# Kernel tuning notes

Measured on AMD Instinct MI355X. Metric: run time of the kernel, lower is better.

The kernel has to match this reference:

```python
import jax, jax.numpy as jnp
import numpy as np

B, T, D, K = 4, 4096, 384, 64

def setup_inputs() -> dict:
    key = jax.random.key(0)
    k1, k2, k3, k4 = jax.random.split(key, 4)
    x = jax.random.normal(k1, (B, T, D), dtype=jnp.float32)
    # nn.Linear weights stored as (out_features, in_features); y = x @ W.T
    Wk = jax.random.normal(k2, (K, D), dtype=jnp.float32) * (1.0 / np.sqrt(D))
    Wq = jax.random.normal(k3, (K, D), dtype=jnp.float32) * (1.0 / np.sqrt(D))
    Wv = jax.random.normal(k4, (D, D), dtype=jnp.float32) * (1.0 / np.sqrt(D))
    return {"x": x, "Wk": Wk, "Wq": Wq, "Wv": Wv}

def reference(x, Wk, Wq, Wv):
    # x: (B,T,D)
    k = jnp.einsum('btd,kd->btk', x, Wk)   # (B,T,K)
    q = jnp.einsum('btd,kd->btk', x, Wq)   # (B,T,K)
    v = jnp.einsum('btd,ed->bte', x, Wv)   # (B,T,D)
    scores = jnp.einsum('btk,bsk->bts', q, k)  # (B,T,T)
    Tq = x.shape[1]
    causal = jnp.tril(jnp.ones((Tq, Tq), dtype=bool))[None, :, :]
    scores = jnp.where(causal, scores, -jnp.inf)
    w = jax.nn.softmax(scores / jnp.sqrt(jnp.asarray(Wk.shape[0], scores.dtype)), axis=-1)
    return jnp.einsum('bts,bsd->btd', w, v)  # (B,T,D)
```

## Files before the change

### kernel.cpp

```cpp
#include <hip/hip_runtime.h>


#define BB 4
#define TT 4096
#define DD 384

#define OWKA 0
#define OWQA 24576
#define OWVB 49152
#define OYK  196608
#define OYQ  1245184
#define OVT  2293760

#define C_EXP 0.18033688011112042f

typedef __bf16 bf16x8 __attribute__((ext_vector_type(8)));
typedef float f32x16 __attribute__((ext_vector_type(16)));
typedef unsigned short u16x4 __attribute__((ext_vector_type(4)));

__device__ __forceinline__ unsigned short f2bf(float f) {
  unsigned int u = __builtin_bit_cast(unsigned int, f);
  u += 0x7FFFu + ((u >> 16) & 1u);
  return (unsigned short)(u >> 16);
}

__device__ __forceinline__ bf16x8 ldb8(const unsigned short* p) {
  return *reinterpret_cast<const bf16x8*>(p);
}

__global__ __launch_bounds__(256) void convert_w(
    const float* __restrict__ Wk, const float* __restrict__ Wq,
    const float* __restrict__ Wv, unsigned short* __restrict__ ws) {
  int g = blockIdx.x * 256 + threadIdx.x;
  int row = g / 96;
  int fin = (g - row * 96) * 4;
  const float* src;
  unsigned short* dstbase;
  int m;
  if (row < 64)       { src = Wk + row * 384;         dstbase = ws + OWKA; m = row; }
  else if (row < 128) { src = Wq + (row - 64) * 384;  dstbase = ws + OWQA; m = row - 64; }
  else                { src = Wv + (row - 128) * 384; dstbase = ws + OWVB; m = row - 128; }
  float4 f = *reinterpret_cast<const float4*>(src + fin);
  u16x4 o;
  o[0] = f2bf(f.x); o[1] = f2bf(f.y); o[2] = f2bf(f.z); o[3] = f2bf(f.w);
  unsigned short* dst = dstbase + (m >> 5) * 12288 + (fin >> 4) * 512
                        + ((((fin >> 3) & 1) << 5) + (m & 31)) * 8 + (fin & 7);
  *reinterpret_cast<u16x4*>(dst) = o;
}

__global__ __launch_bounds__(512) void proj_fused(
    const float* __restrict__ x, const unsigned short* __restrict__ ws_r,
    unsigned short* __restrict__ Yk, unsigned short* __restrict__ Yq,
    unsigned short* __restrict__ Vt) {
  __shared__ __align__(16) unsigned short xlds[24576];
  int tb = blockIdx.x;
  int b = tb >> 6;
  int tid = threadIdx.x;
  {
    int r = tid >> 3, e = tid & 7;
    const float* xr = x + (tb * 64 + r) * DD + e * 48;
#pragma unroll
    for (int i = 0; i < 12; i++) {
      int fin = e * 48 + i * 4;
      float4 f = *reinterpret_cast<const float4*>(xr + i * 4);
      u16x4 o;
      o[0] = f2bf(f.x); o[1] = f2bf(f.y); o[2] = f2bf(f.z); o[3] = f2bf(f.w);
      unsigned short* dst = xlds + (r >> 5) * 12288 + (fin >> 4) * 512
                            + ((((fin >> 3) & 1) << 5) + (r & 31)) * 8 + (fin & 7);
      *reinterpret_cast<u16x4*>(dst) = o;
    }
  }
  __syncthreads();
  int wid = tid >> 6, lane = tid & 63;
  int l31 = lane & 31, h8 = lane >> 5;
  const f32x16 fz16 = {};
  if (wid < 2) {
    const unsigned short* Wa = ws_r + (wid ? OWQA : OWKA) + lane * 8;
    unsigned short* Ysel = (wid ? Yq : Yk);
    f32x16 acc[2][2];
    acc[0][0] = fz16; acc[0][1] = fz16; acc[1][0] = fz16; acc[1][1] = fz16;
    for (int ks = 0; ks < 24; ks++) {
      bf16x8 a0 = ldb8(Wa + ks * 512);
      bf16x8 a1 = ldb8(Wa + 12288 + ks * 512);
      bf16x8 b0 = ldb8(xlds + ks * 512 + lane * 8);
      bf16x8 b1 = ldb8(xlds + 12288 + ks * 512 + lane * 8);
      acc[0][0] = __builtin_amdgcn_mfma_f32_32x32x16_bf16(a0, b0, acc[0][0], 0, 0, 0);
      acc[0][1] = __builtin_amdgcn_mfma_f32_32x32x16_bf16(a0, b1, acc[0][1], 0, 0, 0);
      acc[1][0] = __builtin_amdgcn_mfma_f32_32x32x16_bf16(a1, b0, acc[1][0], 0, 0, 0);
      acc[1][1] = __builtin_amdgcn_mfma_f32_32x32x16_bf16(a1, b1, acc[1][1], 0, 0, 0);
    }
#pragma unroll
    for (int mt = 0; mt < 2; mt++)
#pragma unroll
      for (int nt = 0; nt < 2; nt++) {
        int tile = b * 128 + (tb & 63) * 2 + nt;
#pragma unroll
        for (int rg = 0; rg < 4; rg++) {
          u16x4 o;
#pragma unroll
          for (int i = 0; i < 4; i++) o[i] = f2bf(acc[mt][nt][rg * 4 + i]);
          *reinterpret_cast<u16x4*>(Ysel + tile * 2048 + (mt * 2 + (rg >> 1)) * 512
                                    + (((rg & 1) << 5) + l31) * 8 + 4 * h8) = o;
        }
      }
  } else {
    int vw = wid - 2;
    const unsigned short* Wb = ws_r + OWVB + vw * 2 * 12288 + lane * 8;
    f32x16 acc[2][2];
    acc[0][0] = fz16; acc[0][1] = fz16; acc[1][0] = fz16; acc[1][1] = fz16;
    for (int ks = 0; ks < 24; ks++) {
      bf16x8 a0 = ldb8(xlds + ks * 512 + lane * 8);
      bf16x8 a1 = ldb8(xlds + 12288 + ks * 512 + lane * 8);
      bf16x8 w0 = ldb8(Wb + ks * 512);
      bf16x8 w1 = ldb8(Wb + 12288 + ks * 512);
      acc[0][0] = __builtin_amdgcn_mfma_f32_32x32x16_bf16(a0, w0, acc[0][0], 0, 0, 0);
      acc[0][1] = __builtin_amdgcn_mfma_f32_32x32x16_bf16(a0, w1, acc[0][1], 0, 0, 0);
      acc[1][0] = __builtin_amdgcn_mfma_f32_32x32x16_bf16(a1, w0, acc[1][0], 0, 0, 0);
      acc[1][1] = __builtin_amdgcn_mfma_f32_32x32x16_bf16(a1, w1, acc[1][1], 0, 0, 0);
    }
    int k128 = (tb & 63) >> 1;
#pragma unroll
    for (int t32 = 0; t32 < 2; t32++)
#pragma unroll
      for (int dt = 0; dt < 2; dt++) {
        int dti = vw * 2 + dt;
        unsigned short* vbase = Vt + ((b * 12 + dti) * 32 + k128) * 4096;
#pragma unroll
        for (int rg = 0; rg < 4; rg++) {
          u16x4 o;
#pragma unroll
          for (int i = 0; i < 4; i++) o[i] = f2bf(acc[t32][dt][rg * 4 + i]);
          int kseg = 4 * (tb & 1) + t32 * 2 + (rg >> 1);
          *reinterpret_cast<u16x4*>(vbase + kseg * 512
                                    + (((rg & 1) << 5) + l31) * 8 + 4 * h8) = o;
        }
      }
  }
}

__global__ __launch_bounds__(512, 2) void flash_attn(
    const unsigned short* __restrict__ Yk, const unsigned short* __restrict__ Yq,
    const unsigned short* __restrict__ Vt, float* __restrict__ out) {
  __shared__ __align__(16) unsigned short pbuf[2][2][8192];
  int blk = blockIdx.x;
  int xcd = blk & 7;
  int b = xcd >> 1, half = xcd & 1;
  int n = blk >> 3;
  int st = (n < 32) ? (127 - 2 * n - half) : (2 * (n - 32) + half);
  int tid = threadIdx.x;
  int wid = tid >> 6, lane = tid & 63;
  int g = wid >> 2, wg = wid & 3;
  int l31 = lane & 31, h8 = lane >> 5;
  const f32x16 fz16 = {};
  const unsigned short* qbase = Yq + (b * 128 + st) * 2048 + lane * 8;
  bf16x8 qf[4];
#pragma unroll
  for (int ks = 0; ks < 4; ks++) qf[ks] = ldb8(qbase + ks * 512);
  f32x16 acc[3];
  acc[0] = fz16; acc[1] = fz16; acc[2] = fz16;
  float psum = 0.f;
  int n128 = (st >> 2) + 1;
  int W = (n128 + 1) >> 1;
  int qrow = st * 32 + l31;
  const unsigned short* kbase = Yk + (b * 128 + wg) * 2048 + lane * 8;
  const unsigned short* vbase = Vt + ((b * 12 + wg * 3) * 32) * 4096 + lane * 8;
#pragma unroll 1
  for (int it = 0; it < W; it++) {
    int kb = 2 * it + g;
    int kbc = (kb < n128) ? kb : (n128 - 1);
    const unsigned short* kt = kbase + kbc * 8192;
    bf16x8 kf[4];
#pragma unroll
    for (int ks = 0; ks < 4; ks++) kf[ks] = ldb8(kt + ks * 512);
    f32x16 sacc = fz16;
#pragma unroll
    for (int ks = 0; ks < 4; ks++)
      sacc = __builtin_amdgcn_mfma_f32_32x32x16_bf16(kf[ks], qf[ks], sacc, 0, 0, 0);
    int kg0 = kb * 128 + wg * 32 + 4 * h8;
    unsigned short* pw = pbuf[g][it & 1];
#pragma unroll
    for (int rg = 0; rg < 4; rg++) {
      u16x4 o;
#pragma unroll
      for (int i = 0; i < 4; i++) {
        int key = kg0 + rg * 8 + i;
        float pv = (key > qrow) ? 0.f : exp2f(sacc[rg * 4 + i] * C_EXP);
        psum += pv;
        o[i] = f2bf(pv);
      }
      int gq = wg * 2 + (rg >> 1);
      *reinterpret_cast<u16x4*>(pw + gq * 512 + ((rg & 1) * 32 + l31) * 8 + 4 * h8) = o;
    }
    const unsigned short* vt = vbase + kbc * 4096;
    __syncthreads();
#pragma unroll
    for (int q = 0; q < 8; q++) {
      bf16x8 pfq = ldb8(pw + q * 512 + lane * 8);
      bf16x8 v0 = ldb8(vt + q * 512);
      bf16x8 v1 = ldb8(vt + 32 * 4096 + q * 512);
      bf16x8 v2 = ldb8(vt + 64 * 4096 + q * 512);
      acc[0] = __builtin_amdgcn_mfma_f32_32x32x16_bf16(v0, pfq, acc[0], 0, 0, 0);
      acc[1] = __builtin_amdgcn_mfma_f32_32x32x16_bf16(v1, pfq, acc[1], 0, 0, 0);
      acc[2] = __builtin_amdgcn_mfma_f32_32x32x16_bf16(v2, pfq, acc[2], 0, 0, 0);
    }
  }
  psum += __shfl_xor(psum, 32);
  __syncthreads();
  float* fb = reinterpret_cast<float*>(pbuf);
  if (h8 == 0) fb[12288 + wid * 32 + l31] = psum;
  if (g == 1) {
#pragma unroll
    for (int dt = 0; dt < 3; dt++)
#pragma unroll
      for (int e = 0; e < 16; e++)
        fb[wg * 3072 + (dt * 16 + e) * 64 + lane] = acc[dt][e];
  }
  __syncthreads();
  if (g == 0) {
    float lt = 0.f;
#pragma unroll
    for (int w = 0; w < 8; w++) lt += fb[12288 + w * 32 + l31];
    float inv = 1.0f / lt;
    float* ob = out + (b * TT + st * 32 + l31) * DD + wg * 96;
#pragma unroll
    for (int dt = 0; dt < 3; dt++)
#pragma unroll
      for (int rg = 0; rg < 4; rg++) {
        float4 o4;
        o4.x = (acc[dt][rg * 4 + 0] + fb[wg * 3072 + (dt * 16 + rg * 4 + 0) * 64 + lane]) * inv;
        o4.y = (acc[dt][rg * 4 + 1] + fb[wg * 3072 + (dt * 16 + rg * 4 + 1) * 64 + lane]) * inv;
        o4.z = (acc[dt][rg * 4 + 2] + fb[wg * 3072 + (dt * 16 + rg * 4 + 2) * 64 + lane]) * inv;
        o4.w = (acc[dt][rg * 4 + 3] + fb[wg * 3072 + (dt * 16 + rg * 4 + 3) * 64 + lane]) * inv;
        *reinterpret_cast<float4*>(ob + dt * 32 + rg * 8 + h8 * 4) = o4;
      }
  }
}

extern "C" void kernel_launch(void* const* d_in, const int* in_sizes, int n_in,
                              void* d_out, int out_size, void* d_ws, size_t ws_size,
                              hipStream_t stream) {
  const float* x  = (const float*)d_in[0];
  const float* Wk = (const float*)d_in[1];
  const float* Wq = (const float*)d_in[2];
  const float* Wv = (const float*)d_in[3];
  unsigned short* ws = (unsigned short*)d_ws;
  unsigned short* Yk = ws + OYK;
  unsigned short* Yq = ws + OYQ;
  unsigned short* Vt = ws + OVT;

  convert_w<<<192, 256, 0, stream>>>(Wk, Wq, Wv, ws);
  proj_fused<<<256, 512, 0, stream>>>(x, ws, Yk, Yq, Vt);
  flash_attn<<<512, 512, 0, stream>>>(Yk, Yq, Vt, (float*)d_out);
}
```

Baseline: 164.0 us.

## Keep softmax probabilities in registers via permlane32 swap, drop LDS exchange

Each wave now computes the full 128-key score block itself (4 key sub-tiles) and rearranges the bf16 probabilities into MFMA B-operand layout in registers using permlane32_swap, instead of writing them to shared memory and reading them back after a block-wide barrier. This removes the per-iteration __syncthreads and LDS round-trip. V fragments are prefetched up front, and the final reduction only pairs waves with the same d-slice. The cost is redundant QK^T work across the four d-slice waves and higher register pressure from holding 24 V fragments plus 8 probability fragments.

New measurement: 259.8 us. 1.58x slower.

```diff
diff --git a/kernel.cpp b/kernel.cpp
--- a/kernel.cpp
+++ b/kernel.cpp
@@ -15,8 +15,11 @@
 #define C_EXP 0.18033688011112042f
 
 typedef __bf16 bf16x8 __attribute__((ext_vector_type(8)));
+typedef __bf16 bf16x2v __attribute__((ext_vector_type(2)));
 typedef float f32x16 __attribute__((ext_vector_type(16)));
 typedef unsigned short u16x4 __attribute__((ext_vector_type(4)));
+typedef unsigned int u32x4 __attribute__((ext_vector_type(4)));
+typedef unsigned int u32x2 __attribute__((ext_vector_type(2)));
 
 __device__ __forceinline__ unsigned short f2bf(float f) {
   unsigned int u = __builtin_bit_cast(unsigned int, f);
@@ -141,7 +144,7 @@
 __global__ __launch_bounds__(512, 2) void flash_attn(
     const unsigned short* __restrict__ Yk, const unsigned short* __restrict__ Yq,
     const unsigned short* __restrict__ Vt, float* __restrict__ out) {
-  __shared__ __align__(16) unsigned short pbuf[2][2][8192];
+  __shared__ float fb[4][3136];
   int blk = blockIdx.x;
   int xcd = blk & 7;
   int b = xcd >> 1, half = xcd & 1;
@@ -149,7 +152,7 @@
   int st = (n < 32) ? (127 - 2 * n - half) : (2 * (n - 32) + half);
   int tid = threadIdx.x;
   int wid = tid >> 6, lane = tid & 63;
-  int g = wid >> 2, wg = wid & 3;
+  int g = wid >> 2, ds = wid & 3;
   int l31 = lane & 31, h8 = lane >> 5;
   const f32x16 fz16 = {};
   const unsigned short* qbase = Yq + (b * 128 + st) * 2048 + lane * 8;
@@ -160,77 +163,82 @@
   acc[0] = fz16; acc[1] = fz16; acc[2] = fz16;
   float psum = 0.f;
   int n128 = (st >> 2) + 1;
-  int W = (n128 + 1) >> 1;
   int qrow = st * 32 + l31;
-  const unsigned short* kbase = Yk + (b * 128 + wg) * 2048 + lane * 8;
-  const unsigned short* vbase = Vt + ((b * 12 + wg * 3) * 32) * 4096 + lane * 8;
+  const unsigned short* kbb = Yk + (b * 128) * 2048 + lane * 8;
+  const unsigned short* vbase = Vt + ((b * 12 + ds * 3) * 32) * 4096 + lane * 8;
 #pragma unroll 1
-  for (int it = 0; it < W; it++) {
-    int kb = 2 * it + g;
-    int kbc = (kb < n128) ? kb : (n128 - 1);
-    const unsigned short* kt = kbase + kbc * 8192;
-    bf16x8 kf[4];
-#pragma unroll
-    for (int ks = 0; ks < 4; ks++) kf[ks] = ldb8(kt + ks * 512);
-    f32x16 sacc = fz16;
-#pragma unroll
-    for (int ks = 0; ks < 4; ks++)
-      sacc = __builtin_amdgcn_mfma_f32_32x32x16_bf16(kf[ks], qf[ks], sacc, 0, 0, 0);
-    int kg0 = kb * 128 + wg * 32 + 4 * h8;
-    unsigned short* pw = pbuf[g][it & 1];
-#pragma unroll
-    for (int rg = 0; rg < 4; rg++) {
-      u16x4 o;
-#pragma unroll
-      for (int i = 0; i < 4; i++) {
-        int key = kg0 + rg * 8 + i;
-        float pv = (key > qrow) ? 0.f : exp2f(sacc[rg * 4 + i] * C_EXP);
-        psum += pv;
-        o[i] = f2bf(pv);
-      }
-      int gq = wg * 2 + (rg >> 1);
-      *reinterpret_cast<u16x4*>(pw + gq * 512 + ((rg & 1) * 32 + l31) * 8 + 4 * h8) = o;
-    }
-    const unsigned short* vt = vbase + kbc * 4096;
-    __syncthreads();
+  for (int kb = g; kb < n128; kb += 2) {
+    const unsigned short* vt = vbase + kb * 4096;
+    bf16x8 vf[3][8];
+#pragma unroll
+    for (int dt = 0; dt < 3; dt++)
+#pragma unroll
+      for (int q = 0; q < 8; q++) vf[dt][q] = ldb8(vt + dt * 131072 + q * 512);
+    const unsigned short* kt0 = kbb + kb * 8192;
+    bf16x8 pfr[8];
+#pragma unroll
+    for (int kt = 0; kt < 4; kt++) {
+      bf16x8 k0 = ldb8(kt0 + kt * 2048);
+      bf16x8 k1 = ldb8(kt0 + kt * 2048 + 512);
+      bf16x8 k2 = ldb8(kt0 + kt * 2048 + 1024);
+      bf16x8 k3 = ldb8(kt0 + kt * 2048 + 1536);
+      f32x16 s = fz16;
+      s = __builtin_amdgcn_mfma_f32_32x32x16_bf16(k0, qf[0], s, 0, 0, 0);
+      s = __builtin_amdgcn_mfma_f32_32x32x16_bf16(k1, qf[1], s, 0, 0, 0);
+      s = __builtin_amdgcn_mfma_f32_32x32x16_bf16(k2, qf[2], s, 0, 0, 0);
+      s = __builtin_amdgcn_mfma_f32_32x32x16_bf16(k3, qf[3], s, 0, 0, 0);
+      int kg = kb * 128 + kt * 32 + 4 * h8;
+      unsigned int w[8];
+#pragma unroll
+      for (int i = 0; i < 8; i++) {
+        int r0 = 2 * i;
+        int key0 = kg + (r0 & 3) + 8 * (r0 >> 2);
+        float p0 = (key0 > qrow) ? 0.f : exp2f(s[r0] * C_EXP);
+        float p1 = (key0 + 1 > qrow) ? 0.f : exp2f(s[r0 + 1] * C_EXP);
+        psum += p0 + p1;
+        bf16x2v t; t[0] = (__bf16)p0; t[1] = (__bf16)p1;
+        w[i] = __builtin_bit_cast(unsigned int, t);
+      }
+      u32x2 r0 = __builtin_amdgcn_permlane32_swap(w[0], w[2], false, false);
+      u32x2 r1 = __builtin_amdgcn_permlane32_swap(w[1], w[3], false, false);
+      u32x2 r2 = __builtin_amdgcn_permlane32_swap(w[4], w[6], false, false);
+      u32x2 r3 = __builtin_amdgcn_permlane32_swap(w[5], w[7], false, false);
+      u32x4 f0; f0[0] = r0[0]; f0[1] = r1[0]; f0[2] = r0[1]; f0[3] = r1[1];
+      u32x4 f1; f1[0] = r2[0]; f1[1] = r3[0]; f1[2] = r2[1]; f1[3] = r3[1];
+      pfr[2 * kt] = __builtin_bit_cast(bf16x8, f0);
+      pfr[2 * kt + 1] = __builtin_bit_cast(bf16x8, f1);
+    }
 #pragma unroll
     for (int q = 0; q < 8; q++) {
-      bf16x8 pfq = ldb8(pw + q * 512 + lane * 8);
-      bf16x8 v0 = ldb8(vt + q * 512);
-      bf16x8 v1 = ldb8(vt + 32 * 4096 + q * 512);
-      bf16x8 v2 = ldb8(vt + 64 * 4096 + q * 512);
-      acc[0] = __builtin_amdgcn_mfma_f32_32x32x16_bf16(v0, pfq, acc[0], 0, 0, 0);
-      acc[1] = __builtin_amdgcn_mfma_f32_32x32x16_bf16(v1, pfq, acc[1], 0, 0, 0);
-      acc[2] = __builtin_amdgcn_mfma_f32_32x32x16_bf16(v2, pfq, acc[2], 0, 0, 0);
+      acc[0] = __builtin_amdgcn_mfma_f32_32x32x16_bf16(vf[0][q], pfr[q], acc[0], 0, 0, 0);
+      acc[1] = __builtin_amdgcn_mfma_f32_32x32x16_bf16(vf[1][q], pfr[q], acc[1], 0, 0, 0);
+      acc[2] = __builtin_amdgcn_mfma_f32_32x32x16_bf16(vf[2][q], pfr[q], acc[2], 0, 0, 0);
     }
   }
   psum += __shfl_xor(psum, 32);
-  __syncthreads();
-  float* fb = reinterpret_cast<float*>(pbuf);
-  if (h8 == 0) fb[12288 + wid * 32 + l31] = psum;
   if (g == 1) {
+    float* f = fb[ds];
 #pragma unroll
     for (int dt = 0; dt < 3; dt++)
 #pragma unroll
-      for (int e = 0; e < 16; e++)
-        fb[wg * 3072 + (dt * 16 + e) * 64 + lane] = acc[dt][e];
+      for (int e = 0; e < 16; e++) f[(dt * 16 + e) * 64 + lane] = acc[dt][e];
+    f[3072 + lane] = psum;
   }
   __syncthreads();
   if (g == 0) {
-    float lt = 0.f;
-#pragma unroll
-    for (int w = 0; w < 8; w++) lt += fb[12288 + w * 32 + l31];
+    const float* f = fb[ds];
+    float lt = psum + f[3072 + lane];
     float inv = 1.0f / lt;
-    float* ob = out + (b * TT + st * 32 + l31) * DD + wg * 96;
+    float* ob = out + (b * TT + st * 32 + l31) * DD + ds * 96;
 #pragma unroll
     for (int dt = 0; dt < 3; dt++)
 #pragma unroll
       for (int rg = 0; rg < 4; rg++) {
         float4 o4;
-        o4.x = (acc[dt][rg * 4 + 0] + fb[wg * 3072 + (dt * 16 + rg * 4 + 0) * 64 + lane]) * inv;
-        o4.y = (acc[dt][rg * 4 + 1] + fb[wg * 3072 + (dt * 16 + rg * 4 + 1) * 64 + lane]) * inv;
-        o4.z = (acc[dt][rg * 4 + 2] + fb[wg * 3072 + (dt * 16 + rg * 4 + 2) * 64 + lane]) * inv;
-        o4.w = (acc[dt][rg * 4 + 3] + fb[wg * 3072 + (dt * 16 + rg * 4 + 3) * 64 + lane]) * inv;
+        o4.x = (acc[dt][rg * 4 + 0] + f[(dt * 16 + rg * 4 + 0) * 64 + lane]) * inv;
+        o4.y = (acc[dt][rg * 4 + 1] + f[(dt * 16 + rg * 4 + 1) * 64 + lane]) * inv;
+        o4.z = (acc[dt][rg * 4 + 2] + f[(dt * 16 + rg * 4 + 2) * 64 + lane]) * inv;
+        o4.w = (acc[dt][rg * 4 + 3] + f[(dt * 16 + rg * 4 + 3) * 64 + lane]) * inv;
         *reinterpret_cast<float4*>(ob + dt * 32 + rg * 8 + h8 * 4) = o4;
       }
   }
```
